# Performance work log

Hardware: AMD Instinct MI355X
Metric: run time of the kernel (lower is better)

The kernel has to match this reference:

```python
import jax, jax.numpy as jnp
import numpy as np

EMBED_DIM = 1024
NUM_HEADS = 16
HEAD_DIM = EMBED_DIM // NUM_HEADS


def setup_inputs() -> dict:
    key = jax.random.key(0)
    ks = jax.random.split(key, 9)
    B, S, E = 2, 2048, EMBED_DIM
    scale = 1.0 / np.sqrt(E)
    x = jax.random.normal(ks[0], (B, S, E), dtype=jnp.float32)
    Wq = jax.random.normal(ks[1], (E, E), dtype=jnp.float32) * scale
    bq = jax.random.normal(ks[2], (E,), dtype=jnp.float32) * 0.01
    Wk = jax.random.normal(ks[3], (E, E), dtype=jnp.float32) * scale
    bk = jax.random.normal(ks[4], (E,), dtype=jnp.float32) * 0.01
    Wv = jax.random.normal(ks[5], (E, E), dtype=jnp.float32) * scale
    bv = jax.random.normal(ks[6], (E,), dtype=jnp.float32) * 0.01
    Wo = jax.random.normal(ks[7], (E, E), dtype=jnp.float32) * scale
    bo = jax.random.normal(ks[8], (E,), dtype=jnp.float32) * 0.01
    return {"x": x, "Wq": Wq, "bq": bq, "Wk": Wk, "bk": bk,
            "Wv": Wv, "bv": bv, "Wo": Wo, "bo": bo}


def reference(x, Wq, bq, Wk, bk, Wv, bv, Wo, bo):
    B, S, E = x.shape
    H, D = NUM_HEADS, HEAD_DIM
    # projections (torch Linear: x @ W.T + b), reshape to (B, H, S, D)
    q = (x @ Wq.T + bq).reshape(B, S, H, D).transpose(0, 2, 1, 3)
    k = (x @ Wk.T + bk).reshape(B, S, H, D).transpose(0, 2, 1, 3)
    v = (x @ Wv.T + bv).reshape(B, S, H, D).transpose(0, 2, 1, 3)
    softmax_scale = 1.0 / np.sqrt(D)
    # (B, H, S, S) scores, causal mask, stable softmax
    scores = softmax_scale * jnp.einsum('bhsd,bhtd->bhst', q, k)
    causal = jnp.tril(jnp.ones((S, S), dtype=bool))  # True = keep
    scores = jnp.where(causal, scores, -jnp.inf)
    attn = jax.nn.softmax(scores, axis=-1)
    out = jnp.einsum('bhst,bhtd->bhsd', attn, v)  # (B, H, S, D)
    out = out.transpose(0, 2, 1, 3).reshape(B, S, E)
    return out @ Wo.T + bo
```

## Files before the change

### kernel.cpp

```cpp
#include <hip/hip_runtime.h>
#include <cstdint>
#include <cstddef>

#define SEQ   2048
#define BATCH 2
#define EMB   1024
#define NH    16
#define HD    64
#define MTOT  (BATCH * SEQ)
#define NX    (MTOT * EMB)
#define NW    (EMB * EMB)

typedef __bf16 bf16_t;
typedef __bf16 bf16x4 __attribute__((ext_vector_type(4)));
typedef __bf16 bf16x8 __attribute__((ext_vector_type(8)));
typedef float  f32x4  __attribute__((ext_vector_type(4)));
typedef float  f32x16 __attribute__((ext_vector_type(16)));

typedef __attribute__((address_space(1))) const void* as1cv;
typedef __attribute__((address_space(3))) void*       as3v;

__device__ __forceinline__ void async_cp16(const void* g, void* l) {
  __builtin_amdgcn_global_load_lds((as1cv)g, (as3v)l, 16, 0, 0);
}

__device__ __forceinline__ f32x4 mfma16(bf16x8 a, bf16x8 b, f32x4 c) {
  return __builtin_amdgcn_mfma_f32_16x16x32_bf16(a, b, c, 0, 0, 0);
}
__device__ __forceinline__ f32x16 mfma32(bf16x8 a, bf16x8 b, f32x16 c) {
  return __builtin_amdgcn_mfma_f32_32x32x16_bf16(a, b, c, 0, 0, 0);
}

__global__ __launch_bounds__(256) void cvt_all(
    const float* __restrict__ x,  const float* __restrict__ wq,
    const float* __restrict__ wk, const float* __restrict__ wv,
    const float* __restrict__ wo,
    bf16_t* __restrict__ xb,  bf16_t* __restrict__ wqb,
    bf16_t* __restrict__ wkb, bf16_t* __restrict__ wvb,
    bf16_t* __restrict__ wob) {
  long e = ((long)blockIdx.x * 256 + threadIdx.x) * 4;
  const float* s; bf16_t* d; long off;
  if (e < NX) { s = x; d = xb; off = e; }
  else {
    long e2 = e - NX;
    int w = (int)(e2 >> 20);
    off = e2 & (NW - 1);
    s = (w == 0) ? wq : (w == 1) ? wk : (w == 2) ? wv : wo;
    d = (w == 0) ? wqb : (w == 1) ? wkb : (w == 2) ? wvb : wob;
  }
  float4 v = *(const float4*)(s + off);
  bf16x4 o;
  o[0] = (bf16_t)v.x; o[1] = (bf16_t)v.y; o[2] = (bf16_t)v.z; o[3] = (bf16_t)v.w;
  *(bf16x4*)(d + off) = o;
}

template <typename OT>
__global__ __launch_bounds__(256) void gemm_bt3(
    const bf16_t* __restrict__ A,
    const bf16_t* __restrict__ W0, const bf16_t* __restrict__ W1,
    const bf16_t* __restrict__ W2,
    const float* __restrict__ b0, const float* __restrict__ b1,
    const float* __restrict__ b2,
    OT* __restrict__ C0, OT* __restrict__ C1, OT* __restrict__ C2) {
  constexpr int K = EMB, N = EMB, BK = 32;
  const int z = blockIdx.z;
  const bf16_t* B    = (z == 0) ? W0 : (z == 1) ? W1 : W2;
  const float*  bias = (z == 0) ? b0 : (z == 1) ? b1 : b2;
  OT*           C    = (z == 0) ? C0 : (z == 1) ? C1 : C2;

  __shared__ __align__(16) bf16_t As[128 * BK];
  __shared__ __align__(16) bf16_t Bs[128 * BK];

  const int tid  = threadIdx.x;
  const int lane = tid & 63;
  const int wave = tid >> 6;
  const int quad = lane >> 4;
  const int l16  = lane & 15;
  const int wm   = (wave >> 1) * 64;
  const int wn   = (wave & 1) * 64;
  const int m0   = blockIdx.y * 128;
  const int n0   = blockIdx.x * 128;

  const int c0 = tid, c1 = tid + 256;
  const bf16_t* ga0 = A + (size_t)(m0 + (c0 >> 2)) * K + (c0 & 3) * 8;
  const bf16_t* ga1 = A + (size_t)(m0 + (c1 >> 2)) * K + (c1 & 3) * 8;
  const bf16_t* gb0 = B + (size_t)(n0 + (c0 >> 2)) * K + (c0 & 3) * 8;
  const bf16_t* gb1 = B + (size_t)(n0 + (c1 >> 2)) * K + (c1 & 3) * 8;
  bf16_t* la0 = &As[c0 * 8];
  bf16_t* la1 = &As[c1 * 8];
  bf16_t* lb0 = &Bs[c0 * 8];
  bf16_t* lb1 = &Bs[c1 * 8];

  f32x4 acc[4][4] = {};

  for (int kk = 0; kk < K; kk += BK) {
    async_cp16(ga0 + kk, la0);
    async_cp16(ga1 + kk, la1);
    async_cp16(gb0 + kk, lb0);
    async_cp16(gb1 + kk, lb1);
    __syncthreads();
    bf16x8 af[4], bfr[4];
#pragma unroll
    for (int i = 0; i < 4; ++i)
      af[i] = *(const bf16x8*)&As[(wm + i * 16 + l16) * BK + quad * 8];
#pragma unroll
    for (int j = 0; j < 4; ++j)
      bfr[j] = *(const bf16x8*)&Bs[(wn + j * 16 + l16) * BK + quad * 8];
#pragma unroll
    for (int i = 0; i < 4; ++i)
#pragma unroll
      for (int j = 0; j < 4; ++j)
        acc[i][j] = mfma16(af[i], bfr[j], acc[i][j]);
    __syncthreads();
  }

#pragma unroll
  for (int j = 0; j < 4; ++j) {
    const int col = n0 + wn + j * 16 + l16;
    const float bv = bias[col];
#pragma unroll
    for (int i = 0; i < 4; ++i) {
      const int row = m0 + wm + i * 16 + quad * 4;
#pragma unroll
      for (int r = 0; r < 4; ++r) {
        C[(size_t)(row + r) * N + col] = (OT)(acc[i][j][r] + bv);
      }
    }
  }
}

__global__ __launch_bounds__(256) void attn128(
    const bf16_t* __restrict__ Qg, const bf16_t* __restrict__ Kg,
    const bf16_t* __restrict__ Vg, bf16_t* __restrict__ Og) {
  const int hb  = blockIdx.x;
  const int x   = blockIdx.y;
  const int h   = hb & 15, b = hb >> 4;
  const int tid = threadIdx.x;
  const int lane = tid & 63, wave = tid >> 6;
  const int l31 = lane & 31, hi = lane >> 5;

  __shared__ __align__(16) bf16_t Ks[2][64 * 72];
  __shared__ __align__(16) bf16_t VsT[2][64 * 72];
  __shared__ __align__(16) bf16_t PQ[128 * 72];

  const size_t base = ((size_t)b * SEQ) * EMB + (size_t)h * HD;
  const bf16_t* Kp = Kg + base;
  const bf16_t* Vp = Vg + base;

  const int kr0r = tid >> 3, kcol = (tid & 7) * 8;
  const int kr1r = kr0r + 32;
  const int vt = tid & 63, vd0 = (tid >> 6) * 8;

  bf16_t* Pw = &PQ[wave * (32 * 72)];

  for (int ph = 0; ph < 2; ++ph) {
    const int s   = ph ? (15 - x) : x;
    const int q0  = s * 128;
    const int nit = 2 * s + 2;
    const bf16_t* Qp = Qg + base + (size_t)q0 * EMB;

    uint4 kr0  = *(const uint4*)(Kp + (size_t)kr0r * EMB + kcol);
    uint4 kr1  = *(const uint4*)(Kp + (size_t)kr1r * EMB + kcol);
    bf16x8 vr0 = *(const bf16x8*)(Vp + (size_t)vt * EMB + vd0);
    bf16x8 vr1 = *(const bf16x8*)(Vp + (size_t)vt * EMB + vd0 + 32);

    __syncthreads();
#pragma unroll
    for (int i = 0; i < 4; ++i) {
      const int c = tid + 256 * i;
      *(uint4*)&PQ[(c >> 3) * 72 + (c & 7) * 8] =
          *(const uint4*)(Qp + (size_t)(c >> 3) * EMB + (c & 7) * 8);
    }
    __syncthreads();

    bf16x8 qf[4];
#pragma unroll
    for (int kk = 0; kk < 4; ++kk)
      qf[kk] = *(const bf16x8*)&PQ[(32 * wave + l31) * 72 + kk * 16 + hi * 8];

    f32x16 acc_o0 = {}, acc_o1 = {};
    float l_i[16];
#pragma unroll
    for (int r = 0; r < 16; ++r) l_i[r] = 0.f;

    for (int it = 0; it < nit; ++it) {
      bf16_t* Kc = &Ks[it & 1][0];
      bf16_t* Vc = &VsT[it & 1][0];
      *(uint4*)&Kc[kr0r * 72 + kcol] = kr0;
      *(uint4*)&Kc[kr1r * 72 + kcol] = kr1;
#pragma unroll
      for (int u = 0; u < 8; ++u) {
        Vc[(vd0 + u) * 72 + vt]      = vr0[u];
        Vc[(vd0 + 32 + u) * 72 + vt] = vr1[u];
      }
      __syncthreads();

      if (it + 1 < nit) {
        const bf16_t* Kn = Kp + (size_t)(it + 1) * 64 * EMB;
        const bf16_t* Vn = Vp + (size_t)(it + 1) * 64 * EMB;
        kr0 = *(const uint4*)(Kn + (size_t)kr0r * EMB + kcol);
        kr1 = *(const uint4*)(Kn + (size_t)kr1r * EMB + kcol);
        vr0 = *(const bf16x8*)(Vn + (size_t)vt * EMB + vd0);
        vr1 = *(const bf16x8*)(Vn + (size_t)vt * EMB + vd0 + 32);
      }

      const bool active = (64 * it <= q0 + 32 * wave + 31);
      if (active) {
        f32x16 acc0 = {}, acc1 = {};
#pragma unroll
        for (int kk = 0; kk < 4; ++kk) {
          const bf16x8 kf0 = *(const bf16x8*)&Kc[l31 * 72 + kk * 16 + hi * 8];
          const bf16x8 kf1 =
              *(const bf16x8*)&Kc[(32 + l31) * 72 + kk * 16 + hi * 8];
          acc0 = mfma32(qf[kk], kf0, acc0);
          acc1 = mfma32(qf[kk], kf1, acc1);
        }

        constexpr float SC2 = 0.18033688011112042f;
        if (it >= nit - 2) {
          const int row0 = q0 + 32 * wave + 4 * hi;
          const int c0 = 64 * it + l31, c1 = c0 + 32;
#pragma unroll
          for (int r = 0; r < 16; ++r) {
            const int row = row0 + (r & 3) + 8 * (r >> 2);
            float p0 = exp2f(__builtin_fmaf(acc0[r], SC2, -8.f));
            float p1 = exp2f(__builtin_fmaf(acc1[r], SC2, -8.f));
            if (c0 > row) p0 = 0.f;
            if (c1 > row) p1 = 0.f;
            l_i[r] += p0 + p1;
            const int rl = (r & 3) + 8 * (r >> 2) + 4 * hi;
            Pw[rl * 72 + l31]      = (bf16_t)p0;
            Pw[rl * 72 + 32 + l31] = (bf16_t)p1;
          }
        } else {
#pragma unroll
          for (int r = 0; r < 16; ++r) {
            const float p0 = exp2f(__builtin_fmaf(acc0[r], SC2, -8.f));
            const float p1 = exp2f(__builtin_fmaf(acc1[r], SC2, -8.f));
            l_i[r] += p0 + p1;
            const int rl = (r & 3) + 8 * (r >> 2) + 4 * hi;
            Pw[rl * 72 + l31]      = (bf16_t)p0;
            Pw[rl * 72 + 32 + l31] = (bf16_t)p1;
          }
        }

#pragma unroll
        for (int kk = 0; kk < 4; ++kk) {
          const bf16x8 pf = *(const bf16x8*)&Pw[l31 * 72 + kk * 16 + hi * 8];
          const bf16x8 vf0 = *(const bf16x8*)&Vc[l31 * 72 + kk * 16 + hi * 8];
          const bf16x8 vf1 =
              *(const bf16x8*)&Vc[(32 + l31) * 72 + kk * 16 + hi * 8];
          acc_o0 = mfma32(pf, vf0, acc_o0);
          acc_o1 = mfma32(pf, vf1, acc_o1);
        }
      }
    }

    bf16_t* Op = Og + base + (size_t)(q0 + 32 * wave) * EMB;
#pragma unroll
    for (int r = 0; r < 16; ++r) {
      float rs = l_i[r];
#pragma unroll
      for (int off = 1; off < 32; off <<= 1) rs += __shfl_xor(rs, off, 64);
      const float inv = 1.f / rs;
      const int rl = (r & 3) + 8 * (r >> 2) + 4 * hi;
      Op[(size_t)rl * EMB + l31]      = (bf16_t)(acc_o0[r] * inv);
      Op[(size_t)rl * EMB + 32 + l31] = (bf16_t)(acc_o1[r] * inv);
    }
  }
}

extern "C" void kernel_launch(void* const* d_in, const int* in_sizes, int n_in,
                              void* d_out, int out_size, void* d_ws,
                              size_t ws_size, hipStream_t stream) {
  const float* x  = (const float*)d_in[0];
  const float* Wq = (const float*)d_in[1];
  const float* bq = (const float*)d_in[2];
  const float* Wk = (const float*)d_in[3];
  const float* bk = (const float*)d_in[4];
  const float* Wv = (const float*)d_in[5];
  const float* bv = (const float*)d_in[6];
  const float* Wo = (const float*)d_in[7];
  const float* bo = (const float*)d_in[8];
  float* out = (float*)d_out;

  char* p = (char*)d_ws;
  bf16_t* xb  = (bf16_t*)p; p += (size_t)NX * 2;
  bf16_t* wqb = (bf16_t*)p; p += (size_t)NW * 2;
  bf16_t* wkb = (bf16_t*)p; p += (size_t)NW * 2;
  bf16_t* wvb = (bf16_t*)p; p += (size_t)NW * 2;
  bf16_t* wob = (bf16_t*)p; p += (size_t)NW * 2;
  bf16_t* qb  = (bf16_t*)p; p += (size_t)NX * 2;
  bf16_t* kb  = (bf16_t*)p; p += (size_t)NX * 2;
  bf16_t* vb  = (bf16_t*)p; p += (size_t)NX * 2;
  bf16_t* ab  = (bf16_t*)p; p += (size_t)NX * 2;

  const int ntot = NX + 4 * NW;
  cvt_all<<<dim3(ntot / 4 / 256), 256, 0, stream>>>(
      x, Wq, Wk, Wv, Wo, xb, wqb, wkb, wvb, wob);

  gemm_bt3<bf16_t><<<dim3(EMB / 128, MTOT / 128, 3), 256, 0, stream>>>(
      xb, wqb, wkb, wvb, bq, bk, bv, qb, kb, vb);

  attn128<<<dim3(BATCH * NH, SEQ / 128 / 2), 256, 0, stream>>>(qb, kb, vb, ab);

  gemm_bt3<float><<<dim3(EMB / 128, MTOT / 128, 1), 256, 0, stream>>>(
      ab, wob, wob, wob, bo, bo, bo, out, out, out);
}
```

Measured before the change: 206.7 us.

## Double-buffer GEMM via register prefetch; one query tile per attention block

The GEMM drops direct global-to-LDS async copies in favour of register prefetch into double-buffered LDS tiles. This lets the next K-slice load overlap with the MFMAs and removes the trailing barrier. The attention kernel no longer has each block process a paired short/long query tile. Instead it launches twice as many blocks, one tile each, ordered longest first, to raise parallelism and let the scheduler balance the causal workload. The trade-offs are more registers in the GEMM and unequal per-block work in attention.

```diff
diff --git a/kernel.cpp b/kernel.cpp
--- a/kernel.cpp
+++ b/kernel.cpp
@@ -16,13 +16,6 @@
 typedef __bf16 bf16x8 __attribute__((ext_vector_type(8)));
 typedef float  f32x4  __attribute__((ext_vector_type(4)));
 typedef float  f32x16 __attribute__((ext_vector_type(16)));
-
-typedef __attribute__((address_space(1))) const void* as1cv;
-typedef __attribute__((address_space(3))) void*       as3v;
-
-__device__ __forceinline__ void async_cp16(const void* g, void* l) {
-  __builtin_amdgcn_global_load_lds((as1cv)g, (as3v)l, 16, 0, 0);
-}
 
 __device__ __forceinline__ f32x4 mfma16(bf16x8 a, bf16x8 b, f32x4 c) {
   return __builtin_amdgcn_mfma_f32_16x16x32_bf16(a, b, c, 0, 0, 0);
@@ -68,8 +61,8 @@
   const float*  bias = (z == 0) ? b0 : (z == 1) ? b1 : b2;
   OT*           C    = (z == 0) ? C0 : (z == 1) ? C1 : C2;
 
-  __shared__ __align__(16) bf16_t As[128 * BK];
-  __shared__ __align__(16) bf16_t Bs[128 * BK];
+  __shared__ __align__(16) bf16_t As[2][128 * BK];
+  __shared__ __align__(16) bf16_t Bs[2][128 * BK];
 
   const int tid  = threadIdx.x;
   const int lane = tid & 63;
@@ -86,32 +79,42 @@
   const bf16_t* ga1 = A + (size_t)(m0 + (c1 >> 2)) * K + (c1 & 3) * 8;
   const bf16_t* gb0 = B + (size_t)(n0 + (c0 >> 2)) * K + (c0 & 3) * 8;
   const bf16_t* gb1 = B + (size_t)(n0 + (c1 >> 2)) * K + (c1 & 3) * 8;
-  bf16_t* la0 = &As[c0 * 8];
-  bf16_t* la1 = &As[c1 * 8];
-  bf16_t* lb0 = &Bs[c0 * 8];
-  bf16_t* lb1 = &Bs[c1 * 8];
+  const int lo0 = c0 * 8, lo1 = c1 * 8;
+
+  uint4 ra0 = *(const uint4*)ga0;
+  uint4 ra1 = *(const uint4*)ga1;
+  uint4 rb0 = *(const uint4*)gb0;
+  uint4 rb1 = *(const uint4*)gb1;
 
   f32x4 acc[4][4] = {};
 
   for (int kk = 0; kk < K; kk += BK) {
-    async_cp16(ga0 + kk, la0);
-    async_cp16(ga1 + kk, la1);
-    async_cp16(gb0 + kk, lb0);
-    async_cp16(gb1 + kk, lb1);
+    const int cur = (kk >> 5) & 1;
+    *(uint4*)&As[cur][lo0] = ra0;
+    *(uint4*)&As[cur][lo1] = ra1;
+    *(uint4*)&Bs[cur][lo0] = rb0;
+    *(uint4*)&Bs[cur][lo1] = rb1;
     __syncthreads();
+
+    if (kk + BK < K) {
+      ra0 = *(const uint4*)(ga0 + kk + BK);
+      ra1 = *(const uint4*)(ga1 + kk + BK);
+      rb0 = *(const uint4*)(gb0 + kk + BK);
+      rb1 = *(const uint4*)(gb1 + kk + BK);
+    }
+
     bf16x8 af[4], bfr[4];
 #pragma unroll
     for (int i = 0; i < 4; ++i)
-      af[i] = *(const bf16x8*)&As[(wm + i * 16 + l16) * BK + quad * 8];
+      af[i] = *(const bf16x8*)&As[cur][(wm + i * 16 + l16) * BK + quad * 8];
 #pragma unroll
     for (int j = 0; j < 4; ++j)
-      bfr[j] = *(const bf16x8*)&Bs[(wn + j * 16 + l16) * BK + quad * 8];
+      bfr[j] = *(const bf16x8*)&Bs[cur][(wn + j * 16 + l16) * BK + quad * 8];
 #pragma unroll
     for (int i = 0; i < 4; ++i)
 #pragma unroll
       for (int j = 0; j < 4; ++j)
         acc[i][j] = mfma16(af[i], bfr[j], acc[i][j]);
-    __syncthreads();
   }
 
 #pragma unroll
@@ -133,7 +136,8 @@
     const bf16_t* __restrict__ Qg, const bf16_t* __restrict__ Kg,
     const bf16_t* __restrict__ Vg, bf16_t* __restrict__ Og) {
   const int hb  = blockIdx.x;
-  const int x   = blockIdx.y;
+  const int y   = blockIdx.y;
+  const int s   = (y < 8) ? (15 - y) : (y - 8);
   const int h   = hb & 15, b = hb >> 4;
   const int tid = threadIdx.x;
   const int lane = tid & 63, wave = tid >> 6;
@@ -153,120 +157,116 @@
 
   bf16_t* Pw = &PQ[wave * (32 * 72)];
 
-  for (int ph = 0; ph < 2; ++ph) {
-    const int s   = ph ? (15 - x) : x;
-    const int q0  = s * 128;
-    const int nit = 2 * s + 2;
-    const bf16_t* Qp = Qg + base + (size_t)q0 * EMB;
-
-    uint4 kr0  = *(const uint4*)(Kp + (size_t)kr0r * EMB + kcol);
-    uint4 kr1  = *(const uint4*)(Kp + (size_t)kr1r * EMB + kcol);
-    bf16x8 vr0 = *(const bf16x8*)(Vp + (size_t)vt * EMB + vd0);
-    bf16x8 vr1 = *(const bf16x8*)(Vp + (size_t)vt * EMB + vd0 + 32);
-
+  const int q0  = s * 128;
+  const int nit = 2 * s + 2;
+  const bf16_t* Qp = Qg + base + (size_t)q0 * EMB;
+
+  uint4 kr0  = *(const uint4*)(Kp + (size_t)kr0r * EMB + kcol);
+  uint4 kr1  = *(const uint4*)(Kp + (size_t)kr1r * EMB + kcol);
+  bf16x8 vr0 = *(const bf16x8*)(Vp + (size_t)vt * EMB + vd0);
+  bf16x8 vr1 = *(const bf16x8*)(Vp + (size_t)vt * EMB + vd0 + 32);
+
+#pragma unroll
+  for (int i = 0; i < 4; ++i) {
+    const int c = tid + 256 * i;
+    *(uint4*)&PQ[(c >> 3) * 72 + (c & 7) * 8] =
+        *(const uint4*)(Qp + (size_t)(c >> 3) * EMB + (c & 7) * 8);
+  }
+  __syncthreads();
+
+  bf16x8 qf[4];
+#pragma unroll
+  for (int kk = 0; kk < 4; ++kk)
+    qf[kk] = *(const bf16x8*)&PQ[(32 * wave + l31) * 72 + kk * 16 + hi * 8];
+
+  f32x16 acc_o0 = {}, acc_o1 = {};
+  float l_i[16];
+#pragma unroll
+  for (int r = 0; r < 16; ++r) l_i[r] = 0.f;
+
+  for (int it = 0; it < nit; ++it) {
+    bf16_t* Kc = &Ks[it & 1][0];
+    bf16_t* Vc = &VsT[it & 1][0];
+    *(uint4*)&Kc[kr0r * 72 + kcol] = kr0;
+    *(uint4*)&Kc[kr1r * 72 + kcol] = kr1;
+#pragma unroll
+    for (int u = 0; u < 8; ++u) {
+      Vc[(vd0 + u) * 72 + vt]      = vr0[u];
+      Vc[(vd0 + 32 + u) * 72 + vt] = vr1[u];
+    }
     __syncthreads();
-#pragma unroll
-    for (int i = 0; i < 4; ++i) {
-      const int c = tid + 256 * i;
-      *(uint4*)&PQ[(c >> 3) * 72 + (c & 7) * 8] =
-          *(const uint4*)(Qp + (size_t)(c >> 3) * EMB + (c & 7) * 8);
-    }
-    __syncthreads();
-
-    bf16x8 qf[4];
-#pragma unroll
-    for (int kk = 0; kk < 4; ++kk)
-      qf[kk] = *(const bf16x8*)&PQ[(32 * wave + l31) * 72 + kk * 16 + hi * 8];
-
-    f32x16 acc_o0 = {}, acc_o1 = {};
-    float l_i[16];
-#pragma unroll
-    for (int r = 0; r < 16; ++r) l_i[r] = 0.f;
-
-    for (int it = 0; it < nit; ++it) {
-      bf16_t* Kc = &Ks[it & 1][0];
-      bf16_t* Vc = &VsT[it & 1][0];
-      *(uint4*)&Kc[kr0r * 72 + kcol] = kr0;
-      *(uint4*)&Kc[kr1r * 72 + kcol] = kr1;
-#pragma unroll
-      for (int u = 0; u < 8; ++u) {
-        Vc[(vd0 + u) * 72 + vt]      = vr0[u];
-        Vc[(vd0 + 32 + u) * 72 + vt] = vr1[u];
+
+    if (it + 1 < nit) {
+      const bf16_t* Kn = Kp + (size_t)(it + 1) * 64 * EMB;
+      const bf16_t* Vn = Vp + (size_t)(it + 1) * 64 * EMB;
+      kr0 = *(const uint4*)(Kn + (size_t)kr0r * EMB + kcol);
+      kr1 = *(const uint4*)(Kn + (size_t)kr1r * EMB + kcol);
+      vr0 = *(const bf16x8*)(Vn + (size_t)vt * EMB + vd0);
+      vr1 = *(const bf16x8*)(Vn + (size_t)vt * EMB + vd0 + 32);
+    }
+
+    const bool active = (64 * it <= q0 + 32 * wave + 31);
+    if (active) {
+      f32x16 acc0 = {}, acc1 = {};
+#pragma unroll
+      for (int kk = 0; kk < 4; ++kk) {
+        const bf16x8 kf0 = *(const bf16x8*)&Kc[l31 * 72 + kk * 16 + hi * 8];
+        const bf16x8 kf1 =
+            *(const bf16x8*)&Kc[(32 + l31) * 72 + kk * 16 + hi * 8];
+        acc0 = mfma32(qf[kk], kf0, acc0);
+        acc1 = mfma32(qf[kk], kf1, acc1);
       }
-      __syncthreads();
-
-      if (it + 1 < nit) {
-        const bf16_t* Kn = Kp + (size_t)(it + 1) * 64 * EMB;
-        const bf16_t* Vn = Vp + (size_t)(it + 1) * 64 * EMB;
-        kr0 = *(const uint4*)(Kn + (size_t)kr0r * EMB + kcol);
-        kr1 = *(const uint4*)(Kn + (size_t)kr1r * EMB + kcol);
-        vr0 = *(const bf16x8*)(Vn + (size_t)vt * EMB + vd0);
-        vr1 = *(const bf16x8*)(Vn + (size_t)vt * EMB + vd0 + 32);
-      }
-
-      const bool active = (64 * it <= q0 + 32 * wave + 31);
-      if (active) {
-        f32x16 acc0 = {}, acc1 = {};
-#pragma unroll
-        for (int kk = 0; kk < 4; ++kk) {
-          const bf16x8 kf0 = *(const bf16x8*)&Kc[l31 * 72 + kk * 16 + hi * 8];
-          const bf16x8 kf1 =
-              *(const bf16x8*)&Kc[(32 + l31) * 72 + kk * 16 + hi * 8];
-          acc0 = mfma32(qf[kk], kf0, acc0);
-          acc1 = mfma32(qf[kk], kf1, acc1);
+
+      constexpr float SC2 = 0.18033688011112042f;
+      if (it >= nit - 2) {
+        const int row0 = q0 + 32 * wave + 4 * hi;
+        const int c0 = 64 * it + l31, c1 = c0 + 32;
+#pragma unroll
+        for (int r = 0; r < 16; ++r) {
+          const int row = row0 + (r & 3) + 8 * (r >> 2);
+          float p0 = exp2f(__builtin_fmaf(acc0[r], SC2, -8.f));
+          float p1 = exp2f(__builtin_fmaf(acc1[r], SC2, -8.f));
+          if (c0 > row) p0 = 0.f;
+          if (c1 > row) p1 = 0.f;
+          l_i[r] += p0 + p1;
+          const int rl = (r & 3) + 8 * (r >> 2) + 4 * hi;
+          Pw[rl * 72 + l31]      = (bf16_t)p0;
+          Pw[rl * 72 + 32 + l31] = (bf16_t)p1;
         }
-
-        constexpr float SC2 = 0.18033688011112042f;
-        if (it >= nit - 2) {
-          const int row0 = q0 + 32 * wave + 4 * hi;
-          const int c0 = 64 * it + l31, c1 = c0 + 32;
-#pragma unroll
-          for (int r = 0; r < 16; ++r) {
-            const int row = row0 + (r & 3) + 8 * (r >> 2);
-            float p0 = exp2f(__builtin_fmaf(acc0[r], SC2, -8.f));
-            float p1 = exp2f(__builtin_fmaf(acc1[r], SC2, -8.f));
-            if (c0 > row) p0 = 0.f;
-            if (c1 > row) p1 = 0.f;
-            l_i[r] += p0 + p1;
-            const int rl = (r & 3) + 8 * (r >> 2) + 4 * hi;
-            Pw[rl * 72 + l31]      = (bf16_t)p0;
-            Pw[rl * 72 + 32 + l31] = (bf16_t)p1;
-          }
-        } else {
-#pragma unroll
-          for (int r = 0; r < 16; ++r) {
-            const float p0 = exp2f(__builtin_fmaf(acc0[r], SC2, -8.f));
-            const float p1 = exp2f(__builtin_fmaf(acc1[r], SC2, -8.f));
-            l_i[r] += p0 + p1;
-            const int rl = (r & 3) + 8 * (r >> 2) + 4 * hi;
-            Pw[rl * 72 + l31]      = (bf16_t)p0;
-            Pw[rl * 72 + 32 + l31] = (bf16_t)p1;
-          }
-        }
-
-#pragma unroll
-        for (int kk = 0; kk < 4; ++kk) {
-          const bf16x8 pf = *(const bf16x8*)&Pw[l31 * 72 + kk * 16 + hi * 8];
-          const bf16x8 vf0 = *(const bf16x8*)&Vc[l31 * 72 + kk * 16 + hi * 8];
-          const bf16x8 vf1 =
-              *(const bf16x8*)&Vc[(32 + l31) * 72 + kk * 16 + hi * 8];
-          acc_o0 = mfma32(pf, vf0, acc_o0);
-          acc_o1 = mfma32(pf, vf1, acc_o1);
+      } else {
+#pragma unroll
+        for (int r = 0; r < 16; ++r) {
+          const float p0 = exp2f(__builtin_fmaf(acc0[r], SC2, -8.f));
+          const float p1 = exp2f(__builtin_fmaf(acc1[r], SC2, -8.f));
+          l_i[r] += p0 + p1;
+          const int rl = (r & 3) + 8 * (r >> 2) + 4 * hi;
+          Pw[rl * 72 + l31]      = (bf16_t)p0;
+          Pw[rl * 72 + 32 + l31] = (bf16_t)p1;
         }
       }
-    }
-
-    bf16_t* Op = Og + base + (size_t)(q0 + 32 * wave) * EMB;
-#pragma unroll
-    for (int r = 0; r < 16; ++r) {
-      float rs = l_i[r];
-#pragma unroll
-      for (int off = 1; off < 32; off <<= 1) rs += __shfl_xor(rs, off, 64);
-      const float inv = 1.f / rs;
-      const int rl = (r & 3) + 8 * (r >> 2) + 4 * hi;
-      Op[(size_t)rl * EMB + l31]      = (bf16_t)(acc_o0[r] * inv);
-      Op[(size_t)rl * EMB + 32 + l31] = (bf16_t)(acc_o1[r] * inv);
-    }
+
+#pragma unroll
+      for (int kk = 0; kk < 4; ++kk) {
+        const bf16x8 pf = *(const bf16x8*)&Pw[l31 * 72 + kk * 16 + hi * 8];
+        const bf16x8 vf0 = *(const bf16x8*)&Vc[l31 * 72 + kk * 16 + hi * 8];
+        const bf16x8 vf1 =
+            *(const bf16x8*)&Vc[(32 + l31) * 72 + kk * 16 + hi * 8];
+        acc_o0 = mfma32(pf, vf0, acc_o0);
+        acc_o1 = mfma32(pf, vf1, acc_o1);
+      }
+    }
+  }
+
+  bf16_t* Op = Og + base + (size_t)(q0 + 32 * wave) * EMB;
+#pragma unroll
+  for (int r = 0; r < 16; ++r) {
+    float rs = l_i[r];
+#pragma unroll
+    for (int off = 1; off < 32; off <<= 1) rs += __shfl_xor(rs, off, 64);
+    const float inv = 1.f / rs;
+    const int rl = (r & 3) + 8 * (r >> 2) + 4 * hi;
+    Op[(size_t)rl * EMB + l31]      = (bf16_t)(acc_o0[r] * inv);
+    Op[(size_t)rl * EMB + 32 + l31] = (bf16_t)(acc_o1[r] * inv);
   }
 }
 
@@ -302,7 +302,7 @@
   gemm_bt3<bf16_t><<<dim3(EMB / 128, MTOT / 128, 3), 256, 0, stream>>>(
       xb, wqb, wkb, wvb, bq, bk, bv, qb, kb, vb);
 
-  attn128<<<dim3(BATCH * NH, SEQ / 128 / 2), 256, 0, stream>>>(qb, kb, vb, ab);
+  attn128<<<dim3(BATCH * NH, SEQ / 128), 256, 0, stream>>>(qb, kb, vb, ab);
 
   gemm_bt3<float><<<dim3(EMB / 128, MTOT / 128, 1), 256, 0, stream>>>(
       ab, wob, wob, wob, bo, bo, bo, out, out, out);
```

Result: slower. 215.2 us (+4.1%).
